# Kernel tuning notes

Measured on AMD Instinct MI355X. Metric: run time of the kernel, lower is better.

Reference implementation:

```python
import jax, jax.numpy as jnp
import numpy as np

B, T, D = 4, 2048, 1024
N_HEADS = 16
D_HEAD = D // N_HEADS


def setup_inputs() -> dict:
    key = jax.random.key(0)
    ks = jax.random.split(key, 5)
    s = 1.0 / np.sqrt(D)  # keep activations well-scaled
    return {
        "x": jax.random.normal(ks[0], (B, T, D), dtype=jnp.float32),
        "Wq": jax.random.normal(ks[1], (D, D), dtype=jnp.float32) * s,
        "Wk": jax.random.normal(ks[2], (D, D), dtype=jnp.float32) * s,
        "Wv": jax.random.normal(ks[3], (D, D), dtype=jnp.float32) * s,
        "Wo": jax.random.normal(ks[4], (D, D), dtype=jnp.float32) * s,
    }


def reference(x, Wq, Wk, Wv, Wo):
    Bx, Tx, C = x.shape
    # projections; nn.Linear(d,d,bias=False): y = x @ W^T
    def split_heads(y):
        return y.reshape(Bx, Tx, N_HEADS, D_HEAD).transpose(0, 2, 1, 3)  # [B,H,T,dh]
    q = split_heads(x @ Wq.T)
    k = split_heads(x @ Wk.T)
    v = split_heads(x @ Wv.T)
    scale = 1.0 / np.sqrt(D_HEAD)
    att = jnp.einsum("bhtd,bhsd->bhts", q, k) * scale  # [B,H,T,T]
    causal = jnp.tril(jnp.ones((Tx, Tx), dtype=bool))
    att = jnp.where(causal[None, None], att, -jnp.inf)
    att = jax.nn.softmax(att, axis=-1)
    y = jnp.einsum("bhts,bhsd->bhtd", att, v)  # [B,H,T,dh]
    y = y.transpose(0, 2, 1, 3).reshape(Bx, Tx, C)
    return y @ Wo.T
```

## Files before the change

### kernel.cpp

```cpp
#include <hip/hip_runtime.h>
#include <cstdint>
#include <cstddef>

typedef unsigned short u16;
typedef short bf16x8 __attribute__((ext_vector_type(8)));
typedef unsigned short u16x8 __attribute__((ext_vector_type(8)));
typedef float f32x4 __attribute__((ext_vector_type(4)));
typedef float f32x16 __attribute__((ext_vector_type(16)));
typedef unsigned u32x2 __attribute__((ext_vector_type(2)));

__device__ __forceinline__ u16 f2bf(float x) {
    union { float f; unsigned int u; } v; v.f = x;
    unsigned int u = v.u;
    unsigned int r = (u + 0x7fffu + ((u >> 16) & 1u)) >> 16;
    return (u16)r;
}

__device__ __forceinline__ unsigned cvtpk(float lo, float hi) {
    unsigned r;
    asm("v_cvt_pk_bf16_f32 %0, %1, %2" : "=v"(r) : "v"(lo), "v"(hi));
    return r;
}

__device__ __forceinline__ float exp2v(float x) {
    float y;
    asm("v_exp_f32 %0, %1" : "=v"(y) : "v"(x));
    return y;
}

__device__ __forceinline__ void load_lds16(const void* g, void* l) {
    __builtin_amdgcn_global_load_lds((const __attribute__((address_space(1))) void*)g,
                                     (__attribute__((address_space(3))) void*)l, 16, 0, 0);
}

__global__ void cast_f32_bf16(const float* __restrict__ in, u16* __restrict__ out, int n) {
    int i = (blockIdx.x * blockDim.x + threadIdx.x) * 4;
    int stride = gridDim.x * blockDim.x * 4;
    for (; i < n; i += stride) {
        float4 f = *reinterpret_cast<const float4*>(in + i);
        ushort4 o;
        o.x = f2bf(f.x); o.y = f2bf(f.y); o.z = f2bf(f.z); o.w = f2bf(f.w);
        *reinterpret_cast<ushort4*>(out + i) = o;
    }
}

__global__ void cast_w4(const float* __restrict__ w0, const float* __restrict__ w1,
                        const float* __restrict__ w2, const float* __restrict__ w3,
                        u16* __restrict__ out, int nw) {
    const int wsel = blockIdx.y;
    const float* in = (wsel == 0) ? w0 : (wsel == 1) ? w1 : (wsel == 2) ? w2 : w3;
    u16* o = out + (size_t)wsel * nw;
    int i = (blockIdx.x * blockDim.x + threadIdx.x) * 4;
    int stride = gridDim.x * blockDim.x * 4;
    for (; i < nw; i += stride) {
        float4 f = *reinterpret_cast<const float4*>(in + i);
        ushort4 v;
        v.x = f2bf(f.x); v.y = f2bf(f.y); v.z = f2bf(f.z); v.w = f2bf(f.w);
        *reinterpret_cast<ushort4*>(o + i) = v;
    }
}

__global__ __launch_bounds__(512, 2) void gemm_qkv(const u16* __restrict__ A,
                                                   const u16* __restrict__ Bw,
                                                   u16* __restrict__ qkout,
                                                   u16* __restrict__ vtg) {
    constexpr int K = 1024, NT = 32;
    __shared__ u16 smem[49152];

    const int tid  = threadIdx.x;
    const int m0   = blockIdx.x * 256;
    const int n0   = blockIdx.y * 256;
    const int wid  = tid >> 6, lane = tid & 63;
    const int fr   = lane & 15, g = lane >> 4;
    const int wm   = wid >> 2, wn = wid & 3;

    const int r0   = tid >> 2;
    const int ssrc = (tid & 3) ^ ((r0 >> 1) & 3);
    const int wb   = (tid & ~63) * 8;
    const u16* pA0 = A  + (size_t)(m0 + r0) * K + ssrc * 8;
    const u16* pA1 = A  + (size_t)(m0 + r0 + 128) * K + ssrc * 8;
    const u16* pB0 = Bw + (size_t)(n0 + r0) * K + ssrc * 8;
    const u16* pB1 = Bw + (size_t)(n0 + r0 + 128) * K + ssrc * 8;

    int offA[8], offB[4];
#pragma unroll
    for (int mf = 0; mf < 8; ++mf) {
        const int row = wm * 128 + mf * 16 + fr;
        offA[mf] = row * 32 + (g ^ ((row >> 1) & 3)) * 8;
    }
#pragma unroll
    for (int nfr = 0; nfr < 4; ++nfr) {
        const int row = wn * 64 + nfr * 16 + fr;
        offB[nfr] = 8192 + row * 32 + (g ^ ((row >> 1) & 3)) * 8;
    }

    f32x4 acc[8][4];
#pragma unroll
    for (int i = 0; i < 8; ++i)
#pragma unroll
        for (int j = 0; j < 4; ++j) acc[i][j] = f32x4{0.f, 0.f, 0.f, 0.f};

#define ISSUE(BUF) {                                                   \
        load_lds16(pA0, &smem[(BUF) * 16384 + wb]);                    \
        load_lds16(pA1, &smem[(BUF) * 16384 + 4096 + wb]);             \
        load_lds16(pB0, &smem[(BUF) * 16384 + 8192 + wb]);             \
        load_lds16(pB1, &smem[(BUF) * 16384 + 12288 + wb]);            \
        pA0 += 32; pA1 += 32; pB0 += 32; pB1 += 32; }

    ISSUE(0);
    ISSUE(1);

    int b = 0;
    for (int t = 0; t < NT; ++t) {
        if (t < NT - 1) asm volatile("s_waitcnt vmcnt(4)\n\ts_barrier" ::: "memory");
        else            asm volatile("s_waitcnt vmcnt(0)\n\ts_barrier" ::: "memory");

        if (t + 2 < NT) {
            const int b2 = (b == 0) ? 2 : b - 1;
            ISSUE(b2);
        }

        const u16* Tb = &smem[b * 16384];
        bf16x8 a[8], bv[4];
#pragma unroll
        for (int mf = 0; mf < 8; ++mf)
            a[mf] = *reinterpret_cast<const bf16x8*>(&Tb[offA[mf]]);
#pragma unroll
        for (int nfr = 0; nfr < 4; ++nfr)
            bv[nfr] = *reinterpret_cast<const bf16x8*>(&Tb[offB[nfr]]);

        __builtin_amdgcn_s_setprio(1);
#pragma unroll
        for (int mf = 0; mf < 8; ++mf)
#pragma unroll
            for (int nfr = 0; nfr < 4; ++nfr)
                acc[mf][nfr] = __builtin_amdgcn_mfma_f32_16x16x32_bf16(
                    a[mf], bv[nfr], acc[mf][nfr], 0, 0, 0);
        __builtin_amdgcn_s_setprio(0);

        b = (b == 2) ? 0 : b + 1;
    }
#undef ISSUE

    __syncthreads();

    char* sb = reinterpret_cast<char*>(smem);
    if (n0 < 2048) {
        const float osc = (n0 < 1024) ? 0.18033688011112042f : 1.0f;
#pragma unroll
        for (int half = 0; half < 2; ++half) {
            if (wm == half) {
#pragma unroll
                for (int mf = 0; mf < 8; ++mf)
#pragma unroll
                    for (int nfr = 0; nfr < 4; ++nfr) {
                        const int rl  = mf * 16 + g * 4;
                        const int col = wn * 64 + nfr * 16 + fr;
#pragma unroll
                        for (int i = 0; i < 4; ++i) {
                            const int row  = rl + i;
                            const int byte = row * 512 + ((col * 2) ^ (((row >> 2) & 3) << 5));
                            *reinterpret_cast<u16*>(sb + byte) = f2bf(acc[mf][nfr][i] * osc);
                        }
                    }
            }
            __syncthreads();
            {
                const int row = tid >> 2;
                const int swz = ((row >> 2) & 3) << 5;
#pragma unroll
                for (int p = 0; p < 8; ++p) {
                    const int sl   = (tid & 3) + p * 4;
                    const int byte = row * 512 + ((sl * 16) ^ swz);
                    u16x8 v = *reinterpret_cast<const u16x8*>(sb + byte);
                    *reinterpret_cast<u16x8*>(
                        &qkout[(size_t)(m0 + half * 128 + row) * 2048 + n0 + sl * 8]) = v;
                }
            }
            __syncthreads();
        }
    } else {
        const int bb = m0 >> 11, tloc = m0 & 2047;
#pragma unroll
        for (int half = 0; half < 2; ++half) {
            if ((wn >> 1) == half) {
#pragma unroll
                for (int mf = 0; mf < 8; ++mf)
#pragma unroll
                    for (int nfr = 0; nfr < 4; ++nfr) {
                        const int nl  = (wn & 1) * 64 + nfr * 16 + fr;
                        const int ml0 = wm * 128 + mf * 16 + g * 4;
                        const int f   = ((nl & 3) << 5) | (((nl >> 2) & 1) << 4);
                        uint2 pk;
                        pk.x = cvtpk(acc[mf][nfr][0], acc[mf][nfr][1]);
                        pk.y = cvtpk(acc[mf][nfr][2], acc[mf][nfr][3]);
                        *reinterpret_cast<uint2*>(sb + nl * 512 + ((ml0 * 2) ^ f)) = pk;
                    }
            }
            __syncthreads();
            {
                const int nl = tid >> 2;
                const int f  = ((nl & 3) << 5) | (((nl >> 2) & 1) << 4);
#pragma unroll
                for (int p = 0; p < 8; ++p) {
                    const int sl   = (tid & 3) + p * 4;
                    const int byte = nl * 512 + ((sl * 16) ^ f);
                    u16x8 v = *reinterpret_cast<const u16x8*>(sb + byte);
                    *reinterpret_cast<u16x8*>(
                        &vtg[(size_t)(bb * 1024 + (n0 - 2048) + half * 128 + nl) * 2048 +
                             tloc + sl * 8]) = v;
                }
            }
            __syncthreads();
        }
    }
}

__global__ __launch_bounds__(256) void gemm_out(const u16* __restrict__ A,
                                                const u16* __restrict__ Bw,
                                                float* __restrict__ C,
                                                int M, int N, int K) {
    __shared__ u16 smem[16384];
    u16* As = smem;
    u16* Bs = smem + 4096;

    const int tid  = threadIdx.x;
    const int m0   = blockIdx.x * 128;
    const int n0   = blockIdx.y * 128;
    const int wid  = tid >> 6;
    const int lane = tid & 63;
    const int wr   = (wid >> 1) * 64;
    const int wc   = (wid & 1) * 64;
    const int fr   = lane & 15;
    const int ko   = (lane >> 4) * 8;
    const int rq   = (lane >> 4) * 4;

    f32x4 acc[4][4];
#pragma unroll
    for (int i = 0; i < 4; ++i)
#pragma unroll
        for (int j = 0; j < 4; ++j) acc[i][j] = f32x4{0.f, 0.f, 0.f, 0.f};

    const int lr4 = lane >> 2;
    const int ls  = lane & 3;

    for (int k0 = 0; k0 < K; k0 += 32) {
#pragma unroll
        for (int t = 0; t < 2; ++t) {
            const int qtr = wid * 2 + t;
            const int r   = qtr * 16 + lr4;
            load_lds16(&A[(size_t)(m0 + r) * K + k0 + ls * 8], &As[qtr * 512]);
            load_lds16(&Bw[(size_t)(n0 + r) * K + k0 + ls * 8], &Bs[qtr * 512]);
        }
        __syncthreads();

        bf16x8 af[4], bfr[4];
#pragma unroll
        for (int mf = 0; mf < 4; ++mf)
            af[mf] = *reinterpret_cast<const bf16x8*>(&As[(wr + mf * 16 + fr) * 32 + ko]);
#pragma unroll
        for (int nf = 0; nf < 4; ++nf)
            bfr[nf] = *reinterpret_cast<const bf16x8*>(&Bs[(wc + nf * 16 + fr) * 32 + ko]);
        __builtin_amdgcn_s_setprio(1);
#pragma unroll
        for (int mf = 0; mf < 4; ++mf)
#pragma unroll
            for (int nf = 0; nf < 4; ++nf)
                acc[mf][nf] = __builtin_amdgcn_mfma_f32_16x16x32_bf16(
                    af[mf], bfr[nf], acc[mf][nf], 0, 0, 0);
        __builtin_amdgcn_s_setprio(0);
        __syncthreads();
    }

#pragma unroll
    for (int mf = 0; mf < 4; ++mf)
#pragma unroll
        for (int nf = 0; nf < 4; ++nf)
#pragma unroll
            for (int i = 0; i < 4; ++i)
                C[(size_t)(m0 + wr + mf * 16 + rq + i) * N + n0 + wc + nf * 16 + fr] =
                    acc[mf][nf][i];
}

__global__ __launch_bounds__(512) void attn_fwd(const u16* __restrict__ qk,
                                                const u16* __restrict__ vtg,
                                                u16* __restrict__ Y) {
    constexpr int T = 2048, DQK = 2048, DOUT = 1024;
    const int bh = blockIdx.x;
    const int jb = blockIdx.y;
    const int b  = bh >> 4, hd = bh & 15;
    const int tid = threadIdx.x, w = tid >> 6, lane = tid & 63;
    const int qloc = lane & 31, h2 = lane >> 5;

    __shared__ u16 Ks[2][4096];
    __shared__ u16 Vs[2][4096];

    const size_t rowb = (size_t)b * T;

    const int srow = tid >> 3;
    const int sc   = ((tid & 7) ^ (srow & 7)) * 8;
    const int ldst = w * 512;

    int off[4];
#pragma unroll
    for (int ks = 0; ks < 4; ++ks)
        off[ks] = qloc * 64 + (((2 * ks + h2) ^ (qloc & 7)) * 8);

#define BUILD_PA(sv, RB, dst) {                                               \
        unsigned wa  = cvtpk(sv[RB + 0], sv[RB + 1]);                         \
        unsigned wb2 = cvtpk(sv[RB + 2], sv[RB + 3]);                         \
        unsigned wc2 = cvtpk(sv[RB + 4], sv[RB + 5]);                         \
        unsigned wd  = cvtpk(sv[RB + 6], sv[RB + 7]);                         \
        u32x2 r0 = __builtin_amdgcn_permlane32_swap(wa, wc2, false, false);   \
        u32x2 r1 = __builtin_amdgcn_permlane32_swap(wb2, wd, false, false);   \
        dst.x = r0.x; dst.y = r1.x; dst.z = r0.y; dst.w = r1.y; }

#define PV_STEP(pa, KS, RBOFF, oacc) {                                        \
        bf16x8 vf_ = *reinterpret_cast<const bf16x8*>(&Vb[off[KS] + (RBOFF)]); \
        oacc = __builtin_amdgcn_mfma_f32_32x32x16_bf16(                       \
            *reinterpret_cast<const bf16x8*>(&pa), vf_, oacc, 0, 0, 0); }

    for (int qi = 0; qi < 2; ++qi) {
        const int qt = (qi == 0) ? (7 - jb) : jb;
        const int q0 = qt * 256;
        const int wq = q0 + w * 32;
        const int NT = 4 * qt + 4;

        bf16x8 qf[4];
#pragma unroll
        for (int ks = 0; ks < 4; ++ks)
            qf[ks] = *reinterpret_cast<const bf16x8*>(
                &qk[(rowb + wq + qloc) * DQK + hd * 64 + ks * 16 + h2 * 8]);

        f32x16 o0, o1;
#pragma unroll
        for (int i = 0; i < 16; ++i) { o0[i] = 0.f; o1[i] = 0.f; }
        float lp = 0.f;

        const u16* kp = qk  + (rowb + srow) * DQK + 1024 + hd * 64 + sc;
        const u16* vp = vtg + ((size_t)bh * 64 + srow) * T + sc;

        __syncthreads();

        load_lds16(kp, &Ks[0][ldst]);
        load_lds16(vp, &Vs[0][ldst]);
        kp += 64 * DQK; vp += 64;

        for (int kt = 0; kt < NT; ++kt) {
            __syncthreads();

            if (kt + 1 < NT) {
                const int nb = (kt + 1) & 1;
                load_lds16(kp, &Ks[nb][ldst]);
                load_lds16(vp, &Vs[nb][ldst]);
                kp += 64 * DQK; vp += 64;
            }

            const int k0 = kt * 64;
            if (k0 <= wq + 31) {
                const u16* Kb = Ks[kt & 1];
                const u16* Vb = Vs[kt & 1];
                const bool do1 = (k0 + 32 <= wq + 31);
                const bool dm  = (k0 + 63 > wq);

                f32x16 st0, st1;
#pragma unroll
                for (int i = 0; i < 16; ++i) { st0[i] = 0.f; st1[i] = 0.f; }

                __builtin_amdgcn_s_setprio(1);
#pragma unroll
                for (int ks = 0; ks < 4; ++ks) {
                    bf16x8 kf = *reinterpret_cast<const bf16x8*>(&Kb[off[ks]]);
                    st0 = __builtin_amdgcn_mfma_f32_32x32x16_bf16(kf, qf[ks], st0, 0, 0, 0);
                }
                if (do1) {
#pragma unroll
                    for (int ks = 0; ks < 4; ++ks) {
                        bf16x8 kf = *reinterpret_cast<const bf16x8*>(&Kb[off[ks] + 2048]);
                        st1 = __builtin_amdgcn_mfma_f32_32x32x16_bf16(kf, qf[ks], st1, 0, 0, 0);
                    }
                }
                __builtin_amdgcn_s_setprio(0);

                const int qg = wq + qloc;
#pragma unroll
                for (int i = 0; i < 16; ++i) st0[i] = exp2v(st0[i]);
                if (do1) {
#pragma unroll
                    for (int i = 0; i < 16; ++i) st1[i] = exp2v(st1[i]);
                }
                if (dm) {
#pragma unroll
                    for (int r = 0; r < 16; ++r) {
                        const int crow = (r & 3) + 8 * (r >> 2) + 4 * h2;
                        if (k0 + crow > qg)      st0[r] = 0.f;
                        if (k0 + 32 + crow > qg) st1[r] = 0.f;
                    }
                }
                {
                    float l0 = 0.f, l1 = 0.f, l2 = 0.f, l3 = 0.f;
#pragma unroll
                    for (int i = 0; i < 4; ++i) {
                        l0 += st0[i]; l1 += st0[4 + i]; l2 += st0[8 + i]; l3 += st0[12 + i];
                    }
                    if (do1) {
#pragma unroll
                        for (int i = 0; i < 4; ++i) {
                            l0 += st1[i]; l1 += st1[4 + i]; l2 += st1[8 + i]; l3 += st1[12 + i];
                        }
                    }
                    lp += (l0 + l1) + (l2 + l3);
                }

                uint4 pa0, pa1, pa2, pa3;
                BUILD_PA(st0, 0, pa0);
                BUILD_PA(st0, 8, pa1);
                if (do1) {
                    BUILD_PA(st1, 0, pa2);
                    BUILD_PA(st1, 8, pa3);
                }

                __builtin_amdgcn_s_setprio(1);
                PV_STEP(pa0, 0, 0, o0);
                PV_STEP(pa1, 1, 0, o0);
                PV_STEP(pa0, 0, 2048, o1);
                PV_STEP(pa1, 1, 2048, o1);
                if (do1) {
                    PV_STEP(pa2, 2, 0, o0);
                    PV_STEP(pa3, 3, 0, o0);
                    PV_STEP(pa2, 2, 2048, o1);
                    PV_STEP(pa3, 3, 2048, o1);
                }
                __builtin_amdgcn_s_setprio(0);
            }
        }

        const float lf = lp + __shfl_xor(lp, 32);
        const float linv = 1.0f / lf;
#pragma unroll
        for (int r = 0; r < 16; ++r) {
            const int crow = (r & 3) + 8 * (r >> 2) + 4 * h2;
            const float rl = __shfl(linv, crow);
            const size_t yrow = rowb + wq + crow;
            Y[yrow * DOUT + hd * 64 + qloc]      = (u16)cvtpk(o0[r] * rl, 0.f);
            Y[yrow * DOUT + hd * 64 + 32 + qloc] = (u16)cvtpk(o1[r] * rl, 0.f);
        }
    }
#undef BUILD_PA
#undef PV_STEP
}

extern "C" void kernel_launch(void* const* d_in, const int* in_sizes, int n_in,
                              void* d_out, int out_size, void* d_ws, size_t ws_size,
                              hipStream_t stream) {
    const float* x  = (const float*)d_in[0];
    const float* Wq = (const float*)d_in[1];
    const float* Wk = (const float*)d_in[2];
    const float* Wv = (const float*)d_in[3];
    const float* Wo = (const float*)d_in[4];

    constexpr int B = 4, T = 2048, D = 1024;
    constexpr int M = B * T;
    const int nx = in_sizes[0];
    const int nw = in_sizes[1];

    char* ws = (char*)d_ws;
    u16* xb   = (u16*)(ws);
    u16* qkb  = (u16*)(ws + (16ull << 20));
    u16* vtg  = (u16*)(ws + (48ull << 20));
    u16* yb   = (u16*)(ws + (64ull << 20));
    u16* wqkv = (u16*)(ws + (80ull << 20));
    u16* wob  = wqkv + 3 * (size_t)nw;

    cast_f32_bf16<<<2048, 256, 0, stream>>>(x, xb, nx);
    cast_w4<<<dim3(256, 4), 256, 0, stream>>>(Wq, Wk, Wv, Wo, wqkv, nw);

    gemm_qkv<<<dim3(M / 256, 3072 / 256), 512, 0, stream>>>(xb, wqkv, qkb, vtg);

    attn_fwd<<<dim3(64, 4), 512, 0, stream>>>(qkb, vtg, yb);

    gemm_out<<<dim3(M / 128, D / 128), 256, 0, stream>>>(yb, wob, (float*)d_out, M, D, D);
}
```

Baseline: 167.2 us.

## Shrink GEMM tiles to 128x256, reuse pipelined GEMM for output, split attention blocks

The QKV GEMM moves from 256x256 to 128x256 tiles with a smaller LDS footprint and four blocks per CU, which doubles the grid. The same templated triple-buffered kernel now also handles the output projection, replacing the simpler single-buffered gemm_out. The attention kernel launches one block per (head, query tile) across 512 blocks instead of looping over two paired tiles in each block. It keeps heavy-first ordering for the first 256 blocks. The aim is better occupancy and load balance, at the cost of more redundant weight loads per output tile.

Measured after the change: 150.0 us. 10.3% less time.

```diff
diff --git a/kernel.cpp b/kernel.cpp
--- a/kernel.cpp
+++ b/kernel.cpp
@@ -60,15 +60,16 @@
     }
 }
 
-__global__ __launch_bounds__(512, 2) void gemm_qkv(const u16* __restrict__ A,
-                                                   const u16* __restrict__ Bw,
-                                                   u16* __restrict__ qkout,
-                                                   u16* __restrict__ vtg) {
-    constexpr int K = 1024, NT = 32;
-    __shared__ u16 smem[49152];
+template <int MODE>
+__global__ __launch_bounds__(512, 4) void gemm128(const u16* __restrict__ A,
+                                                  const u16* __restrict__ Bw,
+                                                  void* __restrict__ outp,
+                                                  u16* __restrict__ vtg,
+                                                  int N, int K) {
+    __shared__ u16 smem[36864];
 
     const int tid  = threadIdx.x;
-    const int m0   = blockIdx.x * 256;
+    const int m0   = blockIdx.x * 128;
     const int n0   = blockIdx.y * 256;
     const int wid  = tid >> 6, lane = tid & 63;
     const int fr   = lane & 15, g = lane >> 4;
@@ -76,94 +77,99 @@
 
     const int r0   = tid >> 2;
     const int ssrc = (tid & 3) ^ ((r0 >> 1) & 3);
-    const int wb   = (tid & ~63) * 8;
-    const u16* pA0 = A  + (size_t)(m0 + r0) * K + ssrc * 8;
-    const u16* pA1 = A  + (size_t)(m0 + r0 + 128) * K + ssrc * 8;
+    const int wbu  = (tid & ~63) * 8;
+    const u16* pA  = A  + (size_t)(m0 + r0) * K + ssrc * 8;
     const u16* pB0 = Bw + (size_t)(n0 + r0) * K + ssrc * 8;
     const u16* pB1 = Bw + (size_t)(n0 + r0 + 128) * K + ssrc * 8;
 
-    int offA[8], offB[4];
-#pragma unroll
-    for (int mf = 0; mf < 8; ++mf) {
-        const int row = wm * 128 + mf * 16 + fr;
+    int offA[4], offB[4];
+#pragma unroll
+    for (int mf = 0; mf < 4; ++mf) {
+        const int row = wm * 64 + mf * 16 + fr;
         offA[mf] = row * 32 + (g ^ ((row >> 1) & 3)) * 8;
     }
 #pragma unroll
-    for (int nfr = 0; nfr < 4; ++nfr) {
-        const int row = wn * 64 + nfr * 16 + fr;
-        offB[nfr] = 8192 + row * 32 + (g ^ ((row >> 1) & 3)) * 8;
-    }
-
-    f32x4 acc[8][4];
-#pragma unroll
-    for (int i = 0; i < 8; ++i)
+    for (int nf = 0; nf < 4; ++nf) {
+        const int row = wn * 64 + nf * 16 + fr;
+        offB[nf] = 4096 + row * 32 + (g ^ ((row >> 1) & 3)) * 8;
+    }
+
+    f32x4 acc[4][4];
+#pragma unroll
+    for (int i = 0; i < 4; ++i)
 #pragma unroll
         for (int j = 0; j < 4; ++j) acc[i][j] = f32x4{0.f, 0.f, 0.f, 0.f};
 
 #define ISSUE(BUF) {                                                   \
-        load_lds16(pA0, &smem[(BUF) * 16384 + wb]);                    \
-        load_lds16(pA1, &smem[(BUF) * 16384 + 4096 + wb]);             \
-        load_lds16(pB0, &smem[(BUF) * 16384 + 8192 + wb]);             \
-        load_lds16(pB1, &smem[(BUF) * 16384 + 12288 + wb]);            \
-        pA0 += 32; pA1 += 32; pB0 += 32; pB1 += 32; }
+        load_lds16(pA,  &smem[(BUF) * 12288 + wbu]);                   \
+        load_lds16(pB0, &smem[(BUF) * 12288 + 4096 + wbu]);            \
+        load_lds16(pB1, &smem[(BUF) * 12288 + 8192 + wbu]);            \
+        pA += 32; pB0 += 32; pB1 += 32; }
 
     ISSUE(0);
     ISSUE(1);
 
-    int b = 0;
+    const int NT = K >> 5;
+    int bu = 0;
     for (int t = 0; t < NT; ++t) {
-        if (t < NT - 1) asm volatile("s_waitcnt vmcnt(4)\n\ts_barrier" ::: "memory");
+        if (t < NT - 1) asm volatile("s_waitcnt vmcnt(3)\n\ts_barrier" ::: "memory");
         else            asm volatile("s_waitcnt vmcnt(0)\n\ts_barrier" ::: "memory");
 
         if (t + 2 < NT) {
-            const int b2 = (b == 0) ? 2 : b - 1;
+            const int b2 = (bu == 0) ? 2 : bu - 1;
             ISSUE(b2);
         }
 
-        const u16* Tb = &smem[b * 16384];
-        bf16x8 a[8], bv[4];
-#pragma unroll
-        for (int mf = 0; mf < 8; ++mf)
+        const u16* Tb = &smem[bu * 12288];
+        bf16x8 a[4], bv[4];
+#pragma unroll
+        for (int mf = 0; mf < 4; ++mf)
             a[mf] = *reinterpret_cast<const bf16x8*>(&Tb[offA[mf]]);
 #pragma unroll
-        for (int nfr = 0; nfr < 4; ++nfr)
-            bv[nfr] = *reinterpret_cast<const bf16x8*>(&Tb[offB[nfr]]);
+        for (int nf = 0; nf < 4; ++nf)
+            bv[nf] = *reinterpret_cast<const bf16x8*>(&Tb[offB[nf]]);
 
         __builtin_amdgcn_s_setprio(1);
 #pragma unroll
-        for (int mf = 0; mf < 8; ++mf)
-#pragma unroll
-            for (int nfr = 0; nfr < 4; ++nfr)
-                acc[mf][nfr] = __builtin_amdgcn_mfma_f32_16x16x32_bf16(
-                    a[mf], bv[nfr], acc[mf][nfr], 0, 0, 0);
+        for (int mf = 0; mf < 4; ++mf)
+#pragma unroll
+            for (int nf = 0; nf < 4; ++nf)
+                acc[mf][nf] = __builtin_amdgcn_mfma_f32_16x16x32_bf16(
+                    a[mf], bv[nf], acc[mf][nf], 0, 0, 0);
         __builtin_amdgcn_s_setprio(0);
 
-        b = (b == 2) ? 0 : b + 1;
+        bu = (bu == 2) ? 0 : bu + 1;
     }
 #undef ISSUE
 
-    __syncthreads();
-
-    char* sb = reinterpret_cast<char*>(smem);
-    if (n0 < 2048) {
-        const float osc = (n0 < 1024) ? 0.18033688011112042f : 1.0f;
-#pragma unroll
-        for (int half = 0; half < 2; ++half) {
-            if (wm == half) {
-#pragma unroll
-                for (int mf = 0; mf < 8; ++mf)
-#pragma unroll
-                    for (int nfr = 0; nfr < 4; ++nfr) {
-                        const int rl  = mf * 16 + g * 4;
-                        const int col = wn * 64 + nfr * 16 + fr;
-#pragma unroll
-                        for (int i = 0; i < 4; ++i) {
-                            const int row  = rl + i;
-                            const int byte = row * 512 + ((col * 2) ^ (((row >> 2) & 3) << 5));
-                            *reinterpret_cast<u16*>(sb + byte) = f2bf(acc[mf][nfr][i] * osc);
-                        }
+    if constexpr (MODE == 0) {
+        float* C = (float*)outp;
+#pragma unroll
+        for (int mf = 0; mf < 4; ++mf)
+#pragma unroll
+            for (int nf = 0; nf < 4; ++nf)
+#pragma unroll
+                for (int i = 0; i < 4; ++i)
+                    C[(size_t)(m0 + wm * 64 + mf * 16 + g * 4 + i) * N +
+                      n0 + wn * 64 + nf * 16 + fr] = acc[mf][nf][i];
+    } else {
+        __syncthreads();
+        char* sb = reinterpret_cast<char*>(smem);
+        if (n0 < 2048) {
+            const float osc = (n0 < 1024) ? 0.18033688011112042f : 1.0f;
+            u16* qk = (u16*)outp;
+#pragma unroll
+            for (int mf = 0; mf < 4; ++mf)
+#pragma unroll
+                for (int nf = 0; nf < 4; ++nf) {
+                    const int col = wn * 64 + nf * 16 + fr;
+#pragma unroll
+                    for (int i = 0; i < 4; ++i) {
+                        const int row  = wm * 64 + mf * 16 + g * 4 + i;
+                        const int byte = row * 512 + ((col * 2) ^ (((row >> 2) & 3) << 5));
+                        *reinterpret_cast<u16*>(sb + byte) = f2bf(acc[mf][nf][i] * osc);
                     }
-            }
+                }
             __syncthreads();
             {
                 const int row = tid >> 2;
@@ -174,121 +180,50 @@
                     const int byte = row * 512 + ((sl * 16) ^ swz);
                     u16x8 v = *reinterpret_cast<const u16x8*>(sb + byte);
                     *reinterpret_cast<u16x8*>(
-                        &qkout[(size_t)(m0 + half * 128 + row) * 2048 + n0 + sl * 8]) = v;
-                }
-            }
-            __syncthreads();
-        }
-    } else {
-        const int bb = m0 >> 11, tloc = m0 & 2047;
-#pragma unroll
-        for (int half = 0; half < 2; ++half) {
-            if ((wn >> 1) == half) {
-#pragma unroll
-                for (int mf = 0; mf < 8; ++mf)
-#pragma unroll
-                    for (int nfr = 0; nfr < 4; ++nfr) {
-                        const int nl  = (wn & 1) * 64 + nfr * 16 + fr;
-                        const int ml0 = wm * 128 + mf * 16 + g * 4;
-                        const int f   = ((nl & 3) << 5) | (((nl >> 2) & 1) << 4);
-                        uint2 pk;
-                        pk.x = cvtpk(acc[mf][nfr][0], acc[mf][nfr][1]);
-                        pk.y = cvtpk(acc[mf][nfr][2], acc[mf][nfr][3]);
-                        *reinterpret_cast<uint2*>(sb + nl * 512 + ((ml0 * 2) ^ f)) = pk;
-                    }
-            }
+                        &qk[(size_t)(m0 + row) * 2048 + n0 + sl * 8]) = v;
+                }
+            }
+        } else {
+            const int bb = m0 >> 11, tloc = m0 & 2047;
+#pragma unroll
+            for (int mf = 0; mf < 4; ++mf)
+#pragma unroll
+                for (int nf = 0; nf < 4; ++nf) {
+                    const int nl  = wn * 64 + nf * 16 + fr;
+                    const int ml0 = wm * 64 + mf * 16 + g * 4;
+                    const int f   = (nl & 7) << 5;
+                    uint2 pk;
+                    pk.x = cvtpk(acc[mf][nf][0], acc[mf][nf][1]);
+                    pk.y = cvtpk(acc[mf][nf][2], acc[mf][nf][3]);
+                    *reinterpret_cast<uint2*>(sb + nl * 256 + ((ml0 * 2) ^ f)) = pk;
+                }
             __syncthreads();
             {
-                const int nl = tid >> 2;
-                const int f  = ((nl & 3) << 5) | (((nl >> 2) & 1) << 4);
+                const int nl = tid >> 1;
+                const int f  = (nl & 7) << 5;
 #pragma unroll
                 for (int p = 0; p < 8; ++p) {
-                    const int sl   = (tid & 3) + p * 4;
-                    const int byte = nl * 512 + ((sl * 16) ^ f);
+                    const int sl   = (tid & 1) + p * 2;
+                    const int byte = nl * 256 + ((sl * 16) ^ f);
                     u16x8 v = *reinterpret_cast<const u16x8*>(sb + byte);
                     *reinterpret_cast<u16x8*>(
-                        &vtg[(size_t)(bb * 1024 + (n0 - 2048) + half * 128 + nl) * 2048 +
+                        &vtg[(size_t)(bb * 1024 + (n0 - 2048) + nl) * 2048 +
                              tloc + sl * 8]) = v;
                 }
             }
-            __syncthreads();
         }
     }
 }
 
-__global__ __launch_bounds__(256) void gemm_out(const u16* __restrict__ A,
-                                                const u16* __restrict__ Bw,
-                                                float* __restrict__ C,
-                                                int M, int N, int K) {
-    __shared__ u16 smem[16384];
-    u16* As = smem;
-    u16* Bs = smem + 4096;
-
-    const int tid  = threadIdx.x;
-    const int m0   = blockIdx.x * 128;
-    const int n0   = blockIdx.y * 128;
-    const int wid  = tid >> 6;
-    const int lane = tid & 63;
-    const int wr   = (wid >> 1) * 64;
-    const int wc   = (wid & 1) * 64;
-    const int fr   = lane & 15;
-    const int ko   = (lane >> 4) * 8;
-    const int rq   = (lane >> 4) * 4;
-
-    f32x4 acc[4][4];
-#pragma unroll
-    for (int i = 0; i < 4; ++i)
-#pragma unroll
-        for (int j = 0; j < 4; ++j) acc[i][j] = f32x4{0.f, 0.f, 0.f, 0.f};
-
-    const int lr4 = lane >> 2;
-    const int ls  = lane & 3;
-
-    for (int k0 = 0; k0 < K; k0 += 32) {
-#pragma unroll
-        for (int t = 0; t < 2; ++t) {
-            const int qtr = wid * 2 + t;
-            const int r   = qtr * 16 + lr4;
-            load_lds16(&A[(size_t)(m0 + r) * K + k0 + ls * 8], &As[qtr * 512]);
-            load_lds16(&Bw[(size_t)(n0 + r) * K + k0 + ls * 8], &Bs[qtr * 512]);
-        }
-        __syncthreads();
-
-        bf16x8 af[4], bfr[4];
-#pragma unroll
-        for (int mf = 0; mf < 4; ++mf)
-            af[mf] = *reinterpret_cast<const bf16x8*>(&As[(wr + mf * 16 + fr) * 32 + ko]);
-#pragma unroll
-        for (int nf = 0; nf < 4; ++nf)
-            bfr[nf] = *reinterpret_cast<const bf16x8*>(&Bs[(wc + nf * 16 + fr) * 32 + ko]);
-        __builtin_amdgcn_s_setprio(1);
-#pragma unroll
-        for (int mf = 0; mf < 4; ++mf)
-#pragma unroll
-            for (int nf = 0; nf < 4; ++nf)
-                acc[mf][nf] = __builtin_amdgcn_mfma_f32_16x16x32_bf16(
-                    af[mf], bfr[nf], acc[mf][nf], 0, 0, 0);
-        __builtin_amdgcn_s_setprio(0);
-        __syncthreads();
-    }
-
-#pragma unroll
-    for (int mf = 0; mf < 4; ++mf)
-#pragma unroll
-        for (int nf = 0; nf < 4; ++nf)
-#pragma unroll
-            for (int i = 0; i < 4; ++i)
-                C[(size_t)(m0 + wr + mf * 16 + rq + i) * N + n0 + wc + nf * 16 + fr] =
-                    acc[mf][nf][i];
-}
-
-__global__ __launch_bounds__(512) void attn_fwd(const u16* __restrict__ qk,
-                                                const u16* __restrict__ vtg,
-                                                u16* __restrict__ Y) {
+__global__ __launch_bounds__(512, 4) void attn_fwd(const u16* __restrict__ qk,
+                                                   const u16* __restrict__ vtg,
+                                                   u16* __restrict__ Y) {
     constexpr int T = 2048, DQK = 2048, DOUT = 1024;
-    const int bh = blockIdx.x;
-    const int jb = blockIdx.y;
-    const int b  = bh >> 4, hd = bh & 15;
+    const int idx = blockIdx.x;
+    const int sub = idx & 255;
+    const int bh  = sub & 63;
+    const int qt  = (idx < 256) ? (7 - (sub >> 6)) : (sub >> 6);
+    const int b   = bh >> 4, hd = bh & 15;
     const int tid = threadIdx.x, w = tid >> 6, lane = tid & 63;
     const int qloc = lane & 31, h2 = lane >> 5;
 
@@ -320,131 +255,126 @@
         oacc = __builtin_amdgcn_mfma_f32_32x32x16_bf16(                       \
             *reinterpret_cast<const bf16x8*>(&pa), vf_, oacc, 0, 0, 0); }
 
-    for (int qi = 0; qi < 2; ++qi) {
-        const int qt = (qi == 0) ? (7 - jb) : jb;
-        const int q0 = qt * 256;
-        const int wq = q0 + w * 32;
-        const int NT = 4 * qt + 4;
-
-        bf16x8 qf[4];
-#pragma unroll
-        for (int ks = 0; ks < 4; ++ks)
-            qf[ks] = *reinterpret_cast<const bf16x8*>(
-                &qk[(rowb + wq + qloc) * DQK + hd * 64 + ks * 16 + h2 * 8]);
-
-        f32x16 o0, o1;
-#pragma unroll
-        for (int i = 0; i < 16; ++i) { o0[i] = 0.f; o1[i] = 0.f; }
-        float lp = 0.f;
-
-        const u16* kp = qk  + (rowb + srow) * DQK + 1024 + hd * 64 + sc;
-        const u16* vp = vtg + ((size_t)bh * 64 + srow) * T + sc;
-
+    const int q0 = qt * 256;
+    const int wq = q0 + w * 32;
+    const int NT = 4 * qt + 4;
+
+    bf16x8 qf[4];
+#pragma unroll
+    for (int ks = 0; ks < 4; ++ks)
+        qf[ks] = *reinterpret_cast<const bf16x8*>(
+            &qk[(rowb + wq + qloc) * DQK + hd * 64 + ks * 16 + h2 * 8]);
+
+    f32x16 o0, o1;
+#pragma unroll
+    for (int i = 0; i < 16; ++i) { o0[i] = 0.f; o1[i] = 0.f; }
+    float lp = 0.f;
+
+    const u16* kp = qk  + (rowb + srow) * DQK + 1024 + hd * 64 + sc;
+    const u16* vp = vtg + ((size_t)bh * 64 + srow) * T + sc;
+
+    load_lds16(kp, &Ks[0][ldst]);
+    load_lds16(vp, &Vs[0][ldst]);
+    kp += 64 * DQK; vp += 64;
+
+    for (int kt = 0; kt < NT; ++kt) {
         __syncthreads();
 
-        load_lds16(kp, &Ks[0][ldst]);
-        load_lds16(vp, &Vs[0][ldst]);
-        kp += 64 * DQK; vp += 64;
-
-        for (int kt = 0; kt < NT; ++kt) {
-            __syncthreads();
-
-            if (kt + 1 < NT) {
-                const int nb = (kt + 1) & 1;
-                load_lds16(kp, &Ks[nb][ldst]);
-                load_lds16(vp, &Vs[nb][ldst]);
-                kp += 64 * DQK; vp += 64;
-            }
-
-            const int k0 = kt * 64;
-            if (k0 <= wq + 31) {
-                const u16* Kb = Ks[kt & 1];
-                const u16* Vb = Vs[kt & 1];
-                const bool do1 = (k0 + 32 <= wq + 31);
-                const bool dm  = (k0 + 63 > wq);
-
-                f32x16 st0, st1;
-#pragma unroll
-                for (int i = 0; i < 16; ++i) { st0[i] = 0.f; st1[i] = 0.f; }
-
-                __builtin_amdgcn_s_setprio(1);
+        if (kt + 1 < NT) {
+            const int nb = (kt + 1) & 1;
+            load_lds16(kp, &Ks[nb][ldst]);
+            load_lds16(vp, &Vs[nb][ldst]);
+            kp += 64 * DQK; vp += 64;
+        }
+
+        const int k0 = kt * 64;
+        if (k0 <= wq + 31) {
+            const u16* Kb = Ks[kt & 1];
+            const u16* Vb = Vs[kt & 1];
+            const bool do1 = (k0 + 32 <= wq + 31);
+            const bool dm  = (k0 + 63 > wq);
+
+            f32x16 st0, st1;
+#pragma unroll
+            for (int i = 0; i < 16; ++i) { st0[i] = 0.f; st1[i] = 0.f; }
+
+            __builtin_amdgcn_s_setprio(1);
+#pragma unroll
+            for (int ks = 0; ks < 4; ++ks) {
+                bf16x8 kf = *reinterpret_cast<const bf16x8*>(&Kb[off[ks]]);
+                st0 = __builtin_amdgcn_mfma_f32_32x32x16_bf16(kf, qf[ks], st0, 0, 0, 0);
+            }
+            if (do1) {
 #pragma unroll
                 for (int ks = 0; ks < 4; ++ks) {
-                    bf16x8 kf = *reinterpret_cast<const bf16x8*>(&Kb[off[ks]]);
-                    st0 = __builtin_amdgcn_mfma_f32_32x32x16_bf16(kf, qf[ks], st0, 0, 0, 0);
+                    bf16x8 kf = *reinterpret_cast<const bf16x8*>(&Kb[off[ks] + 2048]);
+                    st1 = __builtin_amdgcn_mfma_f32_32x32x16_bf16(kf, qf[ks], st1, 0, 0, 0);
+                }
+            }
+            __builtin_amdgcn_s_setprio(0);
+
+            const int qg = wq + qloc;
+#pragma unroll
+            for (int i = 0; i < 16; ++i) st0[i] = exp2v(st0[i]);
+            if (do1) {
+#pragma unroll
+                for (int i = 0; i < 16; ++i) st1[i] = exp2v(st1[i]);
+            }
+            if (dm) {
+#pragma unroll
+                for (int r = 0; r < 16; ++r) {
+                    const int crow = (r & 3) + 8 * (r >> 2) + 4 * h2;
+                    if (k0 + crow > qg)      st0[r] = 0.f;
+                    if (k0 + 32 + crow > qg) st1[r] = 0.f;
+                }
+            }
+            {
+                float l0 = 0.f, l1 = 0.f, l2 = 0.f, l3 = 0.f;
+#pragma unroll
+                for (int i = 0; i < 4; ++i) {
+                    l0 += st0[i]; l1 += st0[4 + i]; l2 += st0[8 + i]; l3 += st0[12 + i];
                 }
                 if (do1) {
 #pragma unroll
-                    for (int ks = 0; ks < 4; ++ks) {
-                        bf16x8 kf = *reinterpret_cast<const bf16x8*>(&Kb[off[ks] + 2048]);
-                        st1 = __builtin_amdgcn_mfma_f32_32x32x16_bf16(kf, qf[ks], st1, 0, 0, 0);
+                    for (int i = 0; i < 4; ++i) {
+                        l0 += st1[i]; l1 += st1[4 + i]; l2 += st1[8 + i]; l3 += st1[12 + i];
                     }
                 }
-                __builtin_amdgcn_s_setprio(0);
-
-                const int qg = wq + qloc;
-#pragma unroll
-                for (int i = 0; i < 16; ++i) st0[i] = exp2v(st0[i]);
-                if (do1) {
-#pragma unroll
-                    for (int i = 0; i < 16; ++i) st1[i] = exp2v(st1[i]);
-                }
-                if (dm) {
-#pragma unroll
-                    for (int r = 0; r < 16; ++r) {
-                        const int crow = (r & 3) + 8 * (r >> 2) + 4 * h2;
-                        if (k0 + crow > qg)      st0[r] = 0.f;
-                        if (k0 + 32 + crow > qg) st1[r] = 0.f;
-                    }
-                }
-                {
-                    float l0 = 0.f, l1 = 0.f, l2 = 0.f, l3 = 0.f;
-#pragma unroll
-                    for (int i = 0; i < 4; ++i) {
-                        l0 += st0[i]; l1 += st0[4 + i]; l2 += st0[8 + i]; l3 += st0[12 + i];
-                    }
-                    if (do1) {
-#pragma unroll
-                        for (int i = 0; i < 4; ++i) {
-                            l0 += st1[i]; l1 += st1[4 + i]; l2 += st1[8 + i]; l3 += st1[12 + i];
-                        }
-                    }
-                    lp += (l0 + l1) + (l2 + l3);
-                }
-
-                uint4 pa0, pa1, pa2, pa3;
-                BUILD_PA(st0, 0, pa0);
-                BUILD_PA(st0, 8, pa1);
-                if (do1) {
-                    BUILD_PA(st1, 0, pa2);
-                    BUILD_PA(st1, 8, pa3);
-                }
-
-                __builtin_amdgcn_s_setprio(1);
-                PV_STEP(pa0, 0, 0, o0);
-                PV_STEP(pa1, 1, 0, o0);
-                PV_STEP(pa0, 0, 2048, o1);
-                PV_STEP(pa1, 1, 2048, o1);
-                if (do1) {
-                    PV_STEP(pa2, 2, 0, o0);
-                    PV_STEP(pa3, 3, 0, o0);
-                    PV_STEP(pa2, 2, 2048, o1);
-                    PV_STEP(pa3, 3, 2048, o1);
-                }
-                __builtin_amdgcn_s_setprio(0);
-            }
+                lp += (l0 + l1) + (l2 + l3);
+            }
+
+            uint4 pa0, pa1, pa2, pa3;
+            BUILD_PA(st0, 0, pa0);
+            BUILD_PA(st0, 8, pa1);
+            if (do1) {
+                BUILD_PA(st1, 0, pa2);
+                BUILD_PA(st1, 8, pa3);
+            }
+
+            __builtin_amdgcn_s_setprio(1);
+            PV_STEP(pa0, 0, 0, o0);
+            PV_STEP(pa1, 1, 0, o0);
+            PV_STEP(pa0, 0, 2048, o1);
+            PV_STEP(pa1, 1, 2048, o1);
+            if (do1) {
+                PV_STEP(pa2, 2, 0, o0);
+                PV_STEP(pa3, 3, 0, o0);
+                PV_STEP(pa2, 2, 2048, o1);
+                PV_STEP(pa3, 3, 2048, o1);
+            }
+            __builtin_amdgcn_s_setprio(0);
         }
-
-        const float lf = lp + __shfl_xor(lp, 32);
-        const float linv = 1.0f / lf;
-#pragma unroll
-        for (int r = 0; r < 16; ++r) {
-            const int crow = (r & 3) + 8 * (r >> 2) + 4 * h2;
-            const float rl = __shfl(linv, crow);
-            const size_t yrow = rowb + wq + crow;
-            Y[yrow * DOUT + hd * 64 + qloc]      = (u16)cvtpk(o0[r] * rl, 0.f);
-            Y[yrow * DOUT + hd * 64 + 32 + qloc] = (u16)cvtpk(o1[r] * rl, 0.f);
-        }
+    }
+
+    const float lf = lp + __shfl_xor(lp, 32);
+    const float linv = 1.0f / lf;
+#pragma unroll
+    for (int r = 0; r < 16; ++r) {
+        const int crow = (r & 3) + 8 * (r >> 2) + 4 * h2;
+        const float rl = __shfl(linv, crow);
+        const size_t yrow = rowb + wq + crow;
+        Y[yrow * DOUT + hd * 64 + qloc]      = (u16)cvtpk(o0[r] * rl, 0.f);
+        Y[yrow * DOUT + hd * 64 + 32 + qloc] = (u16)cvtpk(o1[r] * rl, 0.f);
     }
 #undef BUILD_PA
 #undef PV_STEP
@@ -475,9 +405,9 @@
     cast_f32_bf16<<<2048, 256, 0, stream>>>(x, xb, nx);
     cast_w4<<<dim3(256, 4), 256, 0, stream>>>(Wq, Wk, Wv, Wo, wqkv, nw);
 
-    gemm_qkv<<<dim3(M / 256, 3072 / 256), 512, 0, stream>>>(xb, wqkv, qkb, vtg);
-
-    attn_fwd<<<dim3(64, 4), 512, 0, stream>>>(qkb, vtg, yb);
-
-    gemm_out<<<dim3(M / 128, D / 128), 256, 0, stream>>>(yb, wob, (float*)d_out, M, D, D);
-}
+    gemm128<1><<<dim3(M / 128, 3072 / 256), 512, 0, stream>>>(xb, wqkv, qkb, vtg, 3072, D);
+
+    attn_fwd<<<dim3(512), 512, 0, stream>>>(qkb, vtg, yb);
+
+    gemm128<0><<<dim3(M / 128, D / 256), 512, 0, stream>>>(yb, wob, d_out, nullptr, D, D);
+}
```
